# Performance work log

Hardware: AMD Instinct MI355X
Metric: run time of the kernel (lower is better)

Reference implementation:

```python
import jax, jax.numpy as jnp
import numpy as np

B, N_WALLS, N_PARAMS = 2048, 32, 6
INF = jnp.float32(1e9)


def _dist(v):
    # Euclidean norm over last axis
    return jnp.sqrt(jnp.sum(jnp.square(v), axis=-1))


def _side_ratio(a, b):
    smaller = jnp.minimum(a, b)
    bigger = jnp.maximum(a, b)
    safe = jnp.where(bigger > 0.0, bigger, 1.0)
    return jnp.where(bigger > 0.0, smaller / safe, 0.0)


def _bounding_box(start, end, dif, width):
    per = jnp.stack([dif[..., 1], -dif[..., 0]], axis=-1)
    per_dist = _dist(per)[..., None]
    per = jnp.where(per_dist > 0.0, per / jnp.where(per_dist > 0.0, per_dist, 1.0), per)
    per = per * width[..., None] / 2.0
    corners = jnp.stack([start + per, start - per, end + per, end - per], axis=-2)
    right = jnp.max(corners[..., 0], axis=-1)
    top = jnp.max(corners[..., 1], axis=-1)
    center = (start + end) / 2.0
    bb_w = jnp.abs((right - center[..., 0]) * 2.0)
    bb_h = jnp.abs((top - center[..., 1]) * 2.0)
    return bb_w * bb_h, bb_w, bb_h


def _param_distance(pt, pp):
    start_t, start_p = pt[..., :2], pp[..., :2]
    end_t, end_p = pt[..., 2:4], pp[..., 2:4]
    width_t, width_p = pt[..., 4], pp[..., 4]
    dif_t, dif_p = end_t - start_t, end_p - start_p
    center_t, center_p = (start_t + end_t) / 2.0, (start_p + end_p) / 2.0
    len_t, len_p = _dist(dif_t), _dist(dif_p)
    center_d = jnp.square(_dist(center_t - center_p))
    area_t, area_p = len_t * width_t, len_p * width_p
    area_d = jnp.square(area_t - area_p)
    lwr_d = jnp.square(_side_ratio(width_t, len_t) - _side_ratio(width_p, len_p))
    bba_t, bbx_t, bby_t = _bounding_box(start_t, end_t, dif_t, width_t)
    bba_p, bbx_p, bby_p = _bounding_box(start_p, end_p, dif_p, width_p)
    ar_t = jnp.where(bba_t > 0.001, area_t / jnp.where(bba_t > 0.001, bba_t, 1.0), 1.0)
    ar_p = jnp.where(bba_p > 0.001, area_p / jnp.where(bba_p > 0.001, bba_p, 1.0), 1.0)
    rot_d = jnp.square(ar_t - ar_p)
    horiz_d = jnp.square(jnp.abs(bbx_t - bbx_p))
    vert_d = jnp.square(jnp.abs(bby_t - bby_p))
    return area_d + center_d + rot_d + horiz_d + vert_d + lwr_d


def _distance_function(true_mx, pred_mx):
    probs_t = true_mx[..., -1]
    probs_p = pred_mx[..., -1]
    prob_d = jnp.square(probs_t - probs_p)
    param_d = _param_distance(true_mx[..., :-1], pred_mx[..., :-1])
    return 10.0 * prob_d + param_d * probs_t


def _hungarian(cost):
    # Exact minimal-cost assignment (shortest augmenting path / JV), vmapped over batch.
    n = cost.shape[-1]
    rows = jnp.arange(n)

    def solve(c):
        def outer(i0, carry):
            u, v, col4row, row4col = carry
            init = (jnp.int32(i0), jnp.zeros(n, bool), jnp.zeros(n, bool),
                    jnp.full(n, INF), jnp.full(n, -1, jnp.int32),
                    jnp.float32(0.0), jnp.int32(-1))

            def cond(s):
                return s[6] < 0

            def body(s):
                i, SR, SC, spc, path, minVal, sink = s
                SR = SR.at[i].set(True)
                slack = minVal + c[i] - u[i] - v
                better = (~SC) & (slack < spc)
                spc = jnp.where(better, slack, spc)
                path = jnp.where(better, i, path)
                masked = jnp.where(SC, INF, spc)
                j = jnp.argmin(masked).astype(jnp.int32)
                minVal = masked[j]
                SC = SC.at[j].set(True)
                r = row4col[j]
                sink = jnp.where(r < 0, j, jnp.int32(-1))
                return (r, SR, SC, spc, path, minVal, sink)

            _, SR, SC, spc, path, minVal, sink = jax.lax.while_loop(cond, body, init)
            u = u + jnp.where(SR & (rows != i0), minVal - spc[col4row], 0.0)
            u = u.at[i0].add(minVal)
            v = v - jnp.where(SC, minVal - spc, 0.0)

            def aug_cond(s):
                return ~s[3]

            def aug_body(s):
                j, c4r, r4c, _ = s
                i = path[j]
                r4c = r4c.at[j].set(i)
                j_next = c4r[i]
                c4r = c4r.at[i].set(j)
                return (j_next, c4r, r4c, i == i0)

            _, col4row, row4col, _ = jax.lax.while_loop(
                aug_cond, aug_body, (sink, col4row, row4col, False))
            return (u, v, col4row, row4col)

        u, v, col4row, row4col = jax.lax.fori_loop(
            0, n, outer,
            (jnp.zeros(n), jnp.zeros(n), jnp.full(n, -1, jnp.int32), jnp.full(n, -1, jnp.int32)))
        return jnp.zeros((n, n), bool).at[rows, col4row].set(True)

    return jax.vmap(solve)(cost)


def setup_inputs() -> dict:
    key = jax.random.key(0)
    k1, k2 = jax.random.split(key)
    params_true = jax.random.uniform(k1, (B, N_WALLS, N_PARAMS), dtype=jnp.float32)
    params_pred = jax.random.uniform(k2, (B, N_WALLS, N_PARAMS), dtype=jnp.float32)
    return {"params_true": params_true, "params_pred": params_pred}


def reference(params_true, params_pred):
    # pairwise set distance: true varies over axis 1, pred over axis 2
    pred_mx = jnp.broadcast_to(params_pred[:, None, :, :], (B, N_WALLS, N_WALLS, N_PARAMS))
    true_mx = jnp.broadcast_to(params_true[:, :, None, :], (B, N_WALLS, N_WALLS, N_PARAMS))
    edges = _distance_function(true_mx, pred_mx)          # [B, N, N]
    pairing = _hungarian(edges)                           # bool [B, N, N]
    loss = jnp.sum(jnp.where(pairing, edges, 0.0), axis=(1, 2))  # [B]
    return loss
```

## Files before the change

### kernel.cpp

```cpp
#include <hip/hip_runtime.h>

#define NW 32
#define BATCH 2048
#define BIGF 1e9f

template <int CTRL, int ROW_MASK>
__device__ __forceinline__ float dpp_min_step(float x) {
    int xi = __float_as_int(x);
    int ti = __builtin_amdgcn_update_dpp(xi, xi, CTRL, ROW_MASK, 0xF, false);
    return fminf(x, __int_as_float(ti));
}

__device__ __forceinline__ float wave_min64(float x) {
    x = dpp_min_step<0x111, 0xF>(x);
    x = dpp_min_step<0x112, 0xF>(x);
    x = dpp_min_step<0x114, 0xF>(x);
    x = dpp_min_step<0x118, 0xF>(x);
    x = dpp_min_step<0x142, 0xA>(x);
    x = dpp_min_step<0x143, 0xC>(x);
    return __int_as_float(__builtin_amdgcn_readlane(__float_as_int(x), 63));
}

__device__ __forceinline__ float readlane_f(float v, int lane) {
    return __int_as_float(__builtin_amdgcn_readlane(__float_as_int(v), lane));
}

__global__ __launch_bounds__(64) void floorplan_hungarian_kernel(
    const float* __restrict__ params_true,
    const float* __restrict__ params_pred,
    float* __restrict__ out)
{
    const int b    = blockIdx.x;
    const int lane = threadIdx.x;

    __shared__ float cost[NW][NW + 1];
    __shared__ float featT[NW][9];
    __shared__ float featP[NW][9];

    {
        const float* src = (lane < NW)
            ? (params_true + ((size_t)b * NW + lane) * 6)
            : (params_pred + ((size_t)b * NW + (lane - NW)) * 6);
        float sx = src[0], sy = src[1], ex = src[2], ey = src[3];
        float w  = src[4], prob = src[5];

        float dx = ex - sx, dy = ey - sy;
        float cx = (sx + ex) * 0.5f, cy = (sy + ey) * 0.5f;
        float len = sqrtf(dx * dx + dy * dy);
        float area = len * w;

        float smaller = fminf(w, len), bigger = fmaxf(w, len);
        float sr = (bigger > 0.0f) ? (smaller / bigger) : 0.0f;

        float px = dy, py = -dx;
        float pd = len;
        if (pd > 0.0f) { px /= pd; py /= pd; }
        px *= w * 0.5f; py *= w * 0.5f;
        float right = fmaxf(fmaxf(sx + px, sx - px), fmaxf(ex + px, ex - px));
        float top   = fmaxf(fmaxf(sy + py, sy - py), fmaxf(ey + py, ey - py));
        float bbw = fabsf((right - cx) * 2.0f);
        float bbh = fabsf((top   - cy) * 2.0f);
        float bba = bbw * bbh;
        float ar  = (bba > 0.001f) ? (area / bba) : 1.0f;

        float* f = (lane < NW) ? featT[lane] : featP[lane - NW];
        f[0] = cx;  f[1] = cy;  f[2] = area; f[3] = sr;
        f[4] = ar;  f[5] = bbw; f[6] = bbh;  f[7] = prob;
    }
    __syncthreads();

    for (int e = lane; e < NW * NW; e += 64) {
        int i = e >> 5, j = e & 31;
        float dcx = featT[i][0] - featP[j][0];
        float dcy = featT[i][1] - featP[j][1];
        float center_d = dcx * dcx + dcy * dcy;
        float da = featT[i][2] - featP[j][2];   float area_d  = da * da;
        float ds = featT[i][3] - featP[j][3];   float lwr_d   = ds * ds;
        float dr = featT[i][4] - featP[j][4];   float rot_d   = dr * dr;
        float dxw = featT[i][5] - featP[j][5];  float horiz_d = dxw * dxw;
        float dyh = featT[i][6] - featP[j][6];  float vert_d  = dyh * dyh;
        float probt = featT[i][7], probp = featP[j][7];
        float dp = probt - probp;               float prob_d  = dp * dp;
        float param_d = area_d + center_d + rot_d + horiz_d + vert_d + lwr_d;
        cost[i][j] = 10.0f * prob_d + param_d * probt;
    }
    __syncthreads();

    const bool isCol = lane < NW;
    float v_col   = 0.0f;
    float u_row   = 0.0f;
    int   row4col = -1;
    int   col4row = -1;

    for (int i0 = 0; i0 < NW; ++i0) {
        bool  SCb   = !isCol;
        float spc   = BIGF;
        int   path  = -1;
        unsigned srMask = 0;
        float minVal = 0.0f;
        int   i = i0;
        int   sink;

        float cij = cost[i][lane & 31];
        while (true) {
            srMask |= (1u << i);
            float u_i   = readlane_f(u_row, i);
            float slack = minVal + cij - u_i - v_col;
            bool better = (!SCb) && (slack < spc);
            if (better) { spc = slack; path = i; }
            float spcRed = SCb ? BIGF : spc;

            float mv = wave_min64(spcRed);
            unsigned long long hit = __ballot(spcRed == mv);
            int j = __ffsll(hit) - 1;
            minVal = mv;
            if (lane == j) SCb = true;
            int r = __builtin_amdgcn_readlane(row4col, j);
            if (r < 0) { sink = j; break; }
            i = r;
            cij = cost[i][lane & 31];
        }

        {
            int gidx = (col4row < 0) ? 0 : col4row;
            float spc_at_c4r = __shfl(spc, gidx);
            bool in_SR = isCol && ((srMask >> (lane & 31)) & 1u);
            if (lane == i0)              u_row += minVal;
            else if (in_SR)              u_row += minVal - spc_at_c4r;
            if (isCol && SCb)            v_col -= (minVal - spc);
        }

        {
            int j = sink;
            while (true) {
                int ii = __builtin_amdgcn_readlane(path, j);
                if (lane == j) row4col = ii;
                int j_next = __builtin_amdgcn_readlane(col4row, ii);
                if (lane == ii) col4row = j;
                if (ii == i0) break;
                j = j_next;
            }
        }
    }

    float myedge = (isCol && col4row >= 0) ? cost[lane][col4row] : 0.0f;
    #pragma unroll
    for (int off = 32; off >= 1; off >>= 1)
        myedge += __shfl_xor(myedge, off);
    if (lane == 0) out[b] = myedge;
}

extern "C" void kernel_launch(void* const* d_in, const int* in_sizes, int n_in,
                              void* d_out, int out_size, void* d_ws, size_t ws_size,
                              hipStream_t stream) {
    const float* params_true = (const float*)d_in[0];
    const float* params_pred = (const float*)d_in[1];
    float* out = (float*)d_out;
    floorplan_hungarian_kernel<<<BATCH, 64, 0, stream>>>(params_true, params_pred, out);
}
```

Baseline: 139.2 us.

## Cache cost column in registers and shorten wave min reduction to 32 lanes

Each lane preloads its whole cost column into 32 registers and picks cost[i][col] with a uniform-index select tree instead of an LDS read inside the augmenting loop. The wavefront min reduction drops its final row_bcast31 step and reads lane 31, because only lanes 0-31 (columns) carry finite values. This removes LDS latency and one DPP step from the serial critical path. In exchange it adds about 31 selects per iteration and raises register pressure.

Measured after the change: 170.7 us. +22.6%, slower.

```diff
diff --git a/kernel.cpp b/kernel.cpp
--- a/kernel.cpp
+++ b/kernel.cpp
@@ -11,14 +11,13 @@
     return fminf(x, __int_as_float(ti));
 }
 
-__device__ __forceinline__ float wave_min64(float x) {
+__device__ __forceinline__ float wave_min32(float x) {
     x = dpp_min_step<0x111, 0xF>(x);
     x = dpp_min_step<0x112, 0xF>(x);
     x = dpp_min_step<0x114, 0xF>(x);
     x = dpp_min_step<0x118, 0xF>(x);
     x = dpp_min_step<0x142, 0xA>(x);
-    x = dpp_min_step<0x143, 0xC>(x);
-    return __int_as_float(__builtin_amdgcn_readlane(__float_as_int(x), 63));
+    return __int_as_float(__builtin_amdgcn_readlane(__float_as_int(x), 31));
 }
 
 __device__ __forceinline__ float readlane_f(float v, int lane) {
@@ -86,6 +85,14 @@
     }
     __syncthreads();
 
+    const int col = lane & 31;
+#define LOADC(k) const float c##k = cost[k][col];
+    LOADC(0)  LOADC(1)  LOADC(2)  LOADC(3)  LOADC(4)  LOADC(5)  LOADC(6)  LOADC(7)
+    LOADC(8)  LOADC(9)  LOADC(10) LOADC(11) LOADC(12) LOADC(13) LOADC(14) LOADC(15)
+    LOADC(16) LOADC(17) LOADC(18) LOADC(19) LOADC(20) LOADC(21) LOADC(22) LOADC(23)
+    LOADC(24) LOADC(25) LOADC(26) LOADC(27) LOADC(28) LOADC(29) LOADC(30) LOADC(31)
+#undef LOADC
+
     const bool isCol = lane < NW;
     float v_col   = 0.0f;
     float u_row   = 0.0f;
@@ -101,16 +108,34 @@
         int   i = i0;
         int   sink;
 
-        float cij = cost[i][lane & 31];
         while (true) {
             srMask |= (1u << i);
+
+            const bool b0 = i & 1, b1 = i & 2, b2 = i & 4, b3 = i & 8, b4 = i & 16;
+            float a0  = b0 ? c1  : c0;   float a1  = b0 ? c3  : c2;
+            float a2  = b0 ? c5  : c4;   float a3  = b0 ? c7  : c6;
+            float a4  = b0 ? c9  : c8;   float a5  = b0 ? c11 : c10;
+            float a6  = b0 ? c13 : c12;  float a7  = b0 ? c15 : c14;
+            float a8  = b0 ? c17 : c16;  float a9  = b0 ? c19 : c18;
+            float a10 = b0 ? c21 : c20;  float a11 = b0 ? c23 : c22;
+            float a12 = b0 ? c25 : c24;  float a13 = b0 ? c27 : c26;
+            float a14 = b0 ? c29 : c28;  float a15 = b0 ? c31 : c30;
+            float d0 = b1 ? a1  : a0;    float d1 = b1 ? a3  : a2;
+            float d2 = b1 ? a5  : a4;    float d3 = b1 ? a7  : a6;
+            float d4 = b1 ? a9  : a8;    float d5 = b1 ? a11 : a10;
+            float d6 = b1 ? a13 : a12;   float d7 = b1 ? a15 : a14;
+            float e0 = b2 ? d1 : d0;     float e1 = b2 ? d3 : d2;
+            float e2 = b2 ? d5 : d4;     float e3 = b2 ? d7 : d6;
+            float f0 = b3 ? e1 : e0;     float f1 = b3 ? e3 : e2;
+            float cij = b4 ? f1 : f0;
+
             float u_i   = readlane_f(u_row, i);
             float slack = minVal + cij - u_i - v_col;
             bool better = (!SCb) && (slack < spc);
             if (better) { spc = slack; path = i; }
             float spcRed = SCb ? BIGF : spc;
 
-            float mv = wave_min64(spcRed);
+            float mv = wave_min32(spcRed);
             unsigned long long hit = __ballot(spcRed == mv);
             int j = __ffsll(hit) - 1;
             minVal = mv;
@@ -118,7 +143,6 @@
             int r = __builtin_amdgcn_readlane(row4col, j);
             if (r < 0) { sink = j; break; }
             i = r;
-            cij = cost[i][lane & 31];
         }
 
         {
```

## Add LAPJV column reduction and augmenting row reduction before shortest-path phase

Applied to the files above, without the earlier changes.

Before the Hungarian phase, the kernel now runs a Jonker-Volgenant style initialisation. Column reduction seeds the column potentials with each column's minimum cost and assigns those argmin rows. A bounded augmenting row reduction pass (at most 96 steps) then places further free rows using first and second minima. The Dijkstra-style augmenting search runs only for rows still unassigned, and the wave min reduction is cut to 32 lanes because only the column lanes take part. This is meant to cut the number of long serial augmentation loops per batch, at the cost of extra setup work and a riskier potential bookkeeping that must keep reduced costs non-negative.

New measurement: 143.9 us. +3.4%, slower.

```diff
diff --git a/kernel.cpp b/kernel.cpp
--- a/kernel.cpp
+++ b/kernel.cpp
@@ -11,14 +11,13 @@
     return fminf(x, __int_as_float(ti));
 }
 
-__device__ __forceinline__ float wave_min64(float x) {
+__device__ __forceinline__ float wave_min32(float x) {
     x = dpp_min_step<0x111, 0xF>(x);
     x = dpp_min_step<0x112, 0xF>(x);
     x = dpp_min_step<0x114, 0xF>(x);
     x = dpp_min_step<0x118, 0xF>(x);
     x = dpp_min_step<0x142, 0xA>(x);
-    x = dpp_min_step<0x143, 0xC>(x);
-    return __int_as_float(__builtin_amdgcn_readlane(__float_as_int(x), 63));
+    return __int_as_float(__builtin_amdgcn_readlane(__float_as_int(x), 31));
 }
 
 __device__ __forceinline__ float readlane_f(float v, int lane) {
@@ -36,6 +35,7 @@
     __shared__ float cost[NW][NW + 1];
     __shared__ float featT[NW][9];
     __shared__ float featP[NW][9];
+    __shared__ int   rw[NW];
 
     {
         const float* src = (lane < NW)
@@ -69,6 +69,7 @@
     }
     __syncthreads();
 
+    float cmin = BIGF; int cargmin = 0;
     for (int e = lane; e < NW * NW; e += 64) {
         int i = e >> 5, j = e & 31;
         float dcx = featT[i][0] - featP[j][0];
@@ -82,63 +83,122 @@
         float probt = featT[i][7], probp = featP[j][7];
         float dp = probt - probp;               float prob_d  = dp * dp;
         float param_d = area_d + center_d + rot_d + horiz_d + vert_d + lwr_d;
-        cost[i][j] = 10.0f * prob_d + param_d * probt;
-    }
+        float val = 10.0f * prob_d + param_d * probt;
+        cost[i][j] = val;
+        if (val < cmin) { cmin = val; cargmin = i; }
+    }
+    {
+        float om = __shfl_xor(cmin, 32);
+        int   oi = __shfl_xor(cargmin, 32);
+        if (om < cmin || (om == cmin && oi < cargmin)) { cmin = om; cargmin = oi; }
+    }
+    if (lane < NW) rw[lane] = -1;
+    __syncthreads();
+
+    if (lane < NW) rw[cargmin] = lane;
     __syncthreads();
 
     const bool isCol = lane < NW;
-    float v_col   = 0.0f;
+    float v_col   = isCol ? cmin : 0.0f;
     float u_row   = 0.0f;
     int   row4col = -1;
     int   col4row = -1;
-
-    for (int i0 = 0; i0 < NW; ++i0) {
-        bool  SCb   = !isCol;
-        float spc   = BIGF;
-        int   path  = -1;
-        unsigned srMask = 0;
-        float minVal = 0.0f;
-        int   i = i0;
-        int   sink;
-
-        float cij = cost[i][lane & 31];
-        while (true) {
-            srMask |= (1u << i);
-            float u_i   = readlane_f(u_row, i);
-            float slack = minVal + cij - u_i - v_col;
-            bool better = (!SCb) && (slack < spc);
-            if (better) { spc = slack; path = i; }
-            float spcRed = SCb ? BIGF : spc;
-
-            float mv = wave_min64(spcRed);
-            unsigned long long hit = __ballot(spcRed == mv);
-            int j = __ffsll(hit) - 1;
-            minVal = mv;
-            if (lane == j) SCb = true;
-            int r = __builtin_amdgcn_readlane(row4col, j);
-            if (r < 0) { sink = j; break; }
-            i = r;
-            cij = cost[i][lane & 31];
+    if (isCol) {
+        if (rw[lane] >= 0)        col4row = rw[lane];
+        if (rw[cargmin] == lane)  row4col = cargmin;
+    }
+    __syncthreads();
+
+    {
+        unsigned freeRows =
+            (unsigned)(__ballot(isCol && col4row < 0) & 0xffffffffull);
+        int steps = 0;
+        while (freeRows != 0 && steps < 96) {
+            int i = __ffs(freeRows) - 1;
+            freeRows &= (freeRows - 1);
+            bool chain = true;
+            while (chain && steps < 96) {
+                ++steps;
+                float r  = isCol ? (cost[i][lane] - v_col) : BIGF;
+                float m1 = wave_min32(r);
+                unsigned long long h1 = __ballot(r == m1);
+                int j1 = __ffsll(h1) - 1;
+                float r2 = (lane == j1) ? BIGF : r;
+                float m2 = wave_min32(r2);
+
+                int jt = j1;
+                if (m1 < m2) {
+                    if (lane == j1) v_col -= (m2 - m1);
+                } else {
+                    unsigned long long h2 = __ballot(r2 == m2);
+                    int j2 = __ffsll(h2) - 1;
+                    int r4c1 = __builtin_amdgcn_readlane(row4col, j1);
+                    if (r4c1 >= 0) jt = j2;
+                }
+                if (lane == i) u_row = m2;
+
+                int iold = __builtin_amdgcn_readlane(row4col, jt);
+                if (lane == jt)  row4col = i;
+                if (lane == iold) col4row = -1;
+                if (lane == i)   col4row = jt;
+                if (iold >= 0) i = iold; else chain = false;
+            }
         }
-
-        {
-            int gidx = (col4row < 0) ? 0 : col4row;
-            float spc_at_c4r = __shfl(spc, gidx);
-            bool in_SR = isCol && ((srMask >> (lane & 31)) & 1u);
-            if (lane == i0)              u_row += minVal;
-            else if (in_SR)              u_row += minVal - spc_at_c4r;
-            if (isCol && SCb)            v_col -= (minVal - spc);
-        }
-
-        {
-            int j = sink;
+    }
+
+    {
+        unsigned rem = (unsigned)(__ballot(isCol && col4row < 0) & 0xffffffffull);
+        while (rem != 0) {
+            int i0 = __ffs(rem) - 1;
+            rem &= (rem - 1);
+
+            bool  SCb   = !isCol;
+            float spc   = BIGF;
+            int   path  = -1;
+            unsigned srMask = 0;
+            float minVal = 0.0f;
+            int   i = i0;
+            int   sink;
+
+            float cij = isCol ? cost[i][lane] : 0.0f;
             while (true) {
-                int ii = __builtin_amdgcn_readlane(path, j);
-                if (lane == j) row4col = ii;
-                int j_next = __builtin_amdgcn_readlane(col4row, ii);
-                if (lane == ii) col4row = j;
-                if (ii == i0) break;
-                j = j_next;
+                srMask |= (1u << i);
+                float u_i   = readlane_f(u_row, i);
+                float slack = minVal + cij - u_i - v_col;
+                bool better = (!SCb) && (slack < spc);
+                if (better) { spc = slack; path = i; }
+                float spcRed = SCb ? BIGF : spc;
+
+                float mv = wave_min32(spcRed);
+                unsigned long long hit = __ballot(spcRed == mv);
+                int j = __ffsll(hit) - 1;
+                minVal = mv;
+                if (lane == j) SCb = true;
+                int r = __builtin_amdgcn_readlane(row4col, j);
+                if (r < 0) { sink = j; break; }
+                i = r;
+                cij = isCol ? cost[i][lane] : 0.0f;
+            }
+
+            {
+                int gidx = (col4row < 0) ? 0 : col4row;
+                float spc_at_c4r = __shfl(spc, gidx);
+                bool in_SR = isCol && ((srMask >> (lane & 31)) & 1u);
+                if (lane == i0)              u_row += minVal;
+                else if (in_SR)              u_row += minVal - spc_at_c4r;
+                if (isCol && SCb)            v_col -= (minVal - spc);
+            }
+
+            {
+                int j = sink;
+                while (true) {
+                    int ii = __builtin_amdgcn_readlane(path, j);
+                    if (lane == j) row4col = ii;
+                    int j_next = __builtin_amdgcn_readlane(col4row, ii);
+                    if (lane == ii) col4row = j;
+                    if (ii == i0) break;
+                    j = j_next;
+                }
             }
         }
     }
```

## Warm-start Hungarian with column-min greedy assignment and narrow min reduction to 32 lanes

Applied to the files above, without the earlier changes.

Computes each column's minimum cost and its argmin row while the cost matrix is built. It then initializes the column potentials v to those minima and greedily assigns each row to its lowest-index claiming column. Only rows left unassigned go through the augmenting-path search, which should cut the number of outer iterations. The wave min reduction drops its final cross-half step because only the 32 column lanes hold finite values. The risk is correctness: the dual initialization must keep the slack invariants valid and tie-breaking must match the reference assignment. The 32-lane min also assumes that lanes 32-63 never carry a value that matters.

New measurement: 116.6 us. 1.19x faster.

```diff
diff --git a/kernel.cpp b/kernel.cpp
--- a/kernel.cpp
+++ b/kernel.cpp
@@ -11,14 +11,13 @@
     return fminf(x, __int_as_float(ti));
 }
 
-__device__ __forceinline__ float wave_min64(float x) {
+__device__ __forceinline__ float wave_min32(float x) {
     x = dpp_min_step<0x111, 0xF>(x);
     x = dpp_min_step<0x112, 0xF>(x);
     x = dpp_min_step<0x114, 0xF>(x);
     x = dpp_min_step<0x118, 0xF>(x);
     x = dpp_min_step<0x142, 0xA>(x);
-    x = dpp_min_step<0x143, 0xC>(x);
-    return __int_as_float(__builtin_amdgcn_readlane(__float_as_int(x), 63));
+    return __int_as_float(__builtin_amdgcn_readlane(__float_as_int(x), 31));
 }
 
 __device__ __forceinline__ float readlane_f(float v, int lane) {
@@ -36,6 +35,7 @@
     __shared__ float cost[NW][NW + 1];
     __shared__ float featT[NW][9];
     __shared__ float featP[NW][9];
+    __shared__ int   rw[NW];
 
     {
         const float* src = (lane < NW)
@@ -67,8 +67,10 @@
         f[0] = cx;  f[1] = cy;  f[2] = area; f[3] = sr;
         f[4] = ar;  f[5] = bbw; f[6] = bbh;  f[7] = prob;
     }
+    if (lane < NW) rw[lane] = 64;
     __syncthreads();
 
+    float cmin = BIGF; int cargmin = 0;
     for (int e = lane; e < NW * NW; e += 64) {
         int i = e >> 5, j = e & 31;
         float dcx = featT[i][0] - featP[j][0];
@@ -82,63 +84,82 @@
         float probt = featT[i][7], probp = featP[j][7];
         float dp = probt - probp;               float prob_d  = dp * dp;
         float param_d = area_d + center_d + rot_d + horiz_d + vert_d + lwr_d;
-        cost[i][j] = 10.0f * prob_d + param_d * probt;
+        float val = 10.0f * prob_d + param_d * probt;
+        cost[i][j] = val;
+        if (val < cmin) { cmin = val; cargmin = i; }
+    }
+    {
+        float om = __shfl_xor(cmin, 32);
+        int   oi = __shfl_xor(cargmin, 32);
+        if (om < cmin || (om == cmin && oi < cargmin)) { cmin = om; cargmin = oi; }
     }
     __syncthreads();
 
+    if (lane < NW) atomicMin(&rw[cargmin], lane);
+    __syncthreads();
+
     const bool isCol = lane < NW;
-    float v_col   = 0.0f;
+    const int  col   = lane & 31;
+    float v_col   = isCol ? cmin : 0.0f;
     float u_row   = 0.0f;
-    int   row4col = -1;
-    int   col4row = -1;
+    int   win     = isCol ? rw[lane] : 64;
+    int   col4row = (isCol && win < 64) ? win : -1;
+    int   row4col = (isCol && rw[cargmin] == lane) ? cargmin : -1;
+    __syncthreads();
 
-    for (int i0 = 0; i0 < NW; ++i0) {
-        bool  SCb   = !isCol;
-        float spc   = BIGF;
-        int   path  = -1;
-        unsigned srMask = 0;
-        float minVal = 0.0f;
-        int   i = i0;
-        int   sink;
+    {
+        unsigned rem = (unsigned)(__ballot(isCol && col4row < 0) & 0xffffffffull);
+        while (rem != 0) {
+            int i0 = __ffs(rem) - 1;
+            rem &= (rem - 1);
 
-        float cij = cost[i][lane & 31];
-        while (true) {
-            srMask |= (1u << i);
-            float u_i   = readlane_f(u_row, i);
-            float slack = minVal + cij - u_i - v_col;
-            bool better = (!SCb) && (slack < spc);
-            if (better) { spc = slack; path = i; }
-            float spcRed = SCb ? BIGF : spc;
+            bool  SCb   = !isCol;
+            float spc   = BIGF;
+            int   path  = -1;
+            unsigned srMask = 0;
+            float minVal = 0.0f;
+            int   i = i0;
+            int   sink;
 
-            float mv = wave_min64(spcRed);
-            unsigned long long hit = __ballot(spcRed == mv);
-            int j = __ffsll(hit) - 1;
-            minVal = mv;
-            if (lane == j) SCb = true;
-            int r = __builtin_amdgcn_readlane(row4col, j);
-            if (r < 0) { sink = j; break; }
-            i = r;
-            cij = cost[i][lane & 31];
-        }
+            float cij = cost[i][col];
+            while (true) {
+                srMask |= (1u << i);
+                float u_i   = readlane_f(u_row, i);
+                float slack = minVal + cij - u_i - v_col;
+                bool better = (!SCb) && (slack < spc);
+                if (better) { spc = slack; path = i; }
+                float spcRed = SCb ? BIGF : spc;
 
-        {
-            int gidx = (col4row < 0) ? 0 : col4row;
-            float spc_at_c4r = __shfl(spc, gidx);
-            bool in_SR = isCol && ((srMask >> (lane & 31)) & 1u);
-            if (lane == i0)              u_row += minVal;
-            else if (in_SR)              u_row += minVal - spc_at_c4r;
-            if (isCol && SCb)            v_col -= (minVal - spc);
-        }
+                float mv = wave_min32(spcRed);
+                unsigned long long hit = __ballot(spcRed == mv);
+                int j = __ffsll(hit) - 1;
+                minVal = mv;
+                if (lane == j) SCb = true;
+                int r = __builtin_amdgcn_readlane(row4col, j);
+                if (r < 0) { sink = j; break; }
+                i = r;
+                cij = cost[i][col];
+            }
 
-        {
-            int j = sink;
-            while (true) {
-                int ii = __builtin_amdgcn_readlane(path, j);
-                if (lane == j) row4col = ii;
-                int j_next = __builtin_amdgcn_readlane(col4row, ii);
-                if (lane == ii) col4row = j;
-                if (ii == i0) break;
-                j = j_next;
+            {
+                int gidx = (col4row < 0) ? 0 : col4row;
+                float spc_at_c4r = __shfl(spc, gidx);
+                bool in_SR = isCol && ((srMask >> col) & 1u);
+                if (lane == i0)              u_row += minVal;
+                else if (in_SR)              u_row += minVal - spc_at_c4r;
+                if (isCol && SCb)            v_col -= (minVal - spc);
+            }
+
+            {
+                int j = sink;
+                while (true) {
+                    int ii = __builtin_amdgcn_readlane(path, j);
+                    if (lane == j) row4col = ii;
+                    int j_next = __builtin_amdgcn_readlane(col4row, ii);
+                    if (lane == ii) col4row = j;
+                    if (ii == i0) break;
+                    j = j_next;
+                }
             }
         }
     }
```
